# Kernel optimization log

Hardware: AMD Instinct MI355X
Metric: run time of the kernel (lower is better)

The kernel has to match this reference:

```python
import jax, jax.numpy as jnp
import numpy as np

N_NODES = 50000
N_EDGES = 1280000
N_GRAPHS = 64
IN_CH = 6
HID = 64
SLOPE = 0.2  # LeakyReLU negative slope


def _lrelu(x):
    return jax.nn.leaky_relu(x, SLOPE)


def _edge_conv(x, src, dst, W1, b1, W2, b2):
    # PyG EdgeConv: message = nn([x_i, x_j - x_i]); x_i = x[dst], x_j = x[src]; max-aggr onto dst
    xi = x[dst]                                   # [E, F]
    m = jnp.concatenate([xi, x[src] - xi], -1)    # [E, 2F]
    h = _lrelu(_lrelu(m @ W1 + b1) @ W2 + b2)     # [E, H]
    agg = jax.ops.segment_max(h, dst, num_segments=N_NODES)
    return jnp.where(jnp.isneginf(agg), 0.0, agg)  # nodes with no in-edges -> 0


def setup_inputs() -> dict:
    key = jax.random.key(0)
    ks = jax.random.split(key, 12)
    glorot = lambda k, fi, fo: jax.random.normal(k, (fi, fo), jnp.float32) * np.sqrt(2.0 / (fi + fo))
    x = jax.random.normal(ks[0], (N_NODES, IN_CH), jnp.float32)
    edge_index = jax.random.randint(ks[1], (2, N_EDGES), 0, N_NODES, jnp.int64 if jax.config.x64_enabled else jnp.int32)
    batch = jnp.sort(jax.random.randint(ks[2], (N_NODES,), 0, N_GRAPHS))
    return {
        "x": x, "edge_index": edge_index, "batch": batch,
        "W1": glorot(ks[3], 2 * IN_CH, HID), "b1": jnp.zeros((HID,), jnp.float32),
        "W2": glorot(ks[4], HID, HID),       "b2": jnp.zeros((HID,), jnp.float32),
        "W3": glorot(ks[5], 2 * HID, HID),   "b3": jnp.zeros((HID,), jnp.float32),
        "W4": glorot(ks[6], HID, HID),       "b4": jnp.zeros((HID,), jnp.float32),
        "Wc1": glorot(ks[7], 2 * HID, HID),  "bc1": jnp.zeros((HID,), jnp.float32),
        "Wc2": glorot(ks[8], HID, 1),        "bc2": jnp.zeros((1,), jnp.float32),
    }


def reference(x, edge_index, batch, W1, b1, W2, b2, W3, b3, W4, b4, Wc1, bc1, Wc2, bc2):
    src, dst = edge_index[0], edge_index[1]
    h = _edge_conv(x, src, dst, W1, b1, W2, b2)   # [N, H]
    h = _edge_conv(h, src, dst, W3, b3, W4, b4)   # [N, H]
    # global mean + max pool per graph
    cnt = jax.ops.segment_sum(jnp.ones((N_NODES,), h.dtype), batch, num_segments=N_GRAPHS)
    mean_p = jax.ops.segment_sum(h, batch, num_segments=N_GRAPHS) / jnp.clip(cnt, 1.0)[:, None]
    max_p = jax.ops.segment_max(h, batch, num_segments=N_GRAPHS)
    max_p = jnp.where(jnp.isneginf(max_p), 0.0, max_p)
    g = jnp.concatenate([mean_p, max_p], -1)      # [G, 2H]
    logits = _lrelu(g @ Wc1 + bc1) @ Wc2 + bc2    # dropout is identity at inference
    return logits.squeeze(-1)                      # [G]
```

## Files before the change

### kernel.cpp

```cpp
#include <hip/hip_runtime.h>
#include <hip/hip_bf16.h>

#define SLOPE 0.2f
#define NPB 64
#define CAP 2048
#define SUBCAP 384
#define MAXBUCK 1024
#define EPB 4096
#define XF1B 512
#define PPARTS 16

typedef _Float16 f16x8  __attribute__((ext_vector_type(8)));
typedef float    f32x4  __attribute__((ext_vector_type(4)));
typedef unsigned u32;
typedef unsigned u32x4  __attribute__((ext_vector_type(4)));

__device__ __forceinline__ float lrelu(float v) { return fmaxf(v, SLOPE * v); }

__device__ __forceinline__ float lane_bcast(float v, int k) {
    return __int_as_float(__builtin_amdgcn_readlane(__float_as_int(v), k));
}

__device__ __forceinline__ f16x8 lrelu8(f16x8 v) {
    f16x8 s = v * (_Float16)SLOPE;
#if __has_builtin(__builtin_elementwise_max)
    return __builtin_elementwise_max(v, s);
#else
    f16x8 r;
#pragma unroll
    for (int i = 0; i < 8; ++i) r[i] = v[i] > s[i] ? v[i] : s[i];
    return r;
#endif
}

__device__ __forceinline__ void split_f16(float v, _Float16& h, _Float16& l) {
    h = (_Float16)v;
    l = (_Float16)(v - (float)h);
}
__device__ __forceinline__ u32 pack_f16(_Float16 a, _Float16 b) {
    return (u32)__builtin_bit_cast(unsigned short, a) |
           ((u32)__builtin_bit_cast(unsigned short, b) << 16);
}

__global__ void __launch_bounds__(256) scatter_xform1_kernel(
    const int* __restrict__ srcI, const int* __restrict__ dstI,
    int* __restrict__ cursor, u32* __restrict__ pairW,
    int E, int nNodes, int nBuck, int nCntB,
    const float* __restrict__ x,
    const float* __restrict__ W1, const float* __restrict__ b1,
    _Float16* __restrict__ Ph, _Float16* __restrict__ Qh)
{
    if (blockIdx.x < nCntB) {
        __shared__ int cnt4[4][MAXBUCK];
        __shared__ int base[MAXBUCK];
        const int tid = threadIdx.x;
        const int wv  = tid >> 6;
        const int j   = blockIdx.x & 7;
        const int e0 = blockIdx.x * EPB;
        const int e1 = min(e0 + EPB, E);
        const int n4 = (e1 - e0) >> 2;
        const int4* d4 = (const int4*)(dstI + e0);
        const int4* s4 = (const int4*)(srcI + e0);

        for (int b = tid; b < nBuck; b += 256) {
            cnt4[0][b] = 0; cnt4[1][b] = 0; cnt4[2][b] = 0; cnt4[3][b] = 0;
        }
        __syncthreads();
        int* mycnt = cnt4[wv];
        for (int i = tid; i < n4; i += 256) {
            const int4 d = d4[i];
            atomicAdd(&mycnt[d.x >> 6], 1);
            atomicAdd(&mycnt[d.y >> 6], 1);
            atomicAdd(&mycnt[d.z >> 6], 1);
            atomicAdd(&mycnt[d.w >> 6], 1);
        }
        for (int e = e0 + (n4 << 2) + tid; e < e1; e += 256)
            atomicAdd(&mycnt[dstI[e] >> 6], 1);
        __syncthreads();
        for (int b = tid; b < nBuck; b += 256) {
            const int c = (cnt4[0][b] + cnt4[1][b]) + (cnt4[2][b] + cnt4[3][b]);
            base[b] = (c > 0)
                ? ((b * 8 + j) * SUBCAP + min(atomicAdd(&cursor[b * 8 + j], c), SUBCAP))
                : 0;
        }
        __syncthreads();
        for (int b = tid; b < nBuck; b += 256) cnt4[0][b] = 0;
        __syncthreads();
        int* scnt = cnt4[0];
        for (int i = tid; i < n4; i += 256) {
            const int4 d = d4[i];
            const int4 s = s4[i];
            {
                const int b = d.x >> 6;
                const int loc = atomicAdd(&scnt[b], 1);
                pairW[min(base[b] + loc, (b * 8 + j + 1) * SUBCAP - 1)] =
                    ((u32)s.x << 6) | (u32)(d.x & (NPB - 1));
            }
            {
                const int b = d.y >> 6;
                const int loc = atomicAdd(&scnt[b], 1);
                pairW[min(base[b] + loc, (b * 8 + j + 1) * SUBCAP - 1)] =
                    ((u32)s.y << 6) | (u32)(d.y & (NPB - 1));
            }
            {
                const int b = d.z >> 6;
                const int loc = atomicAdd(&scnt[b], 1);
                pairW[min(base[b] + loc, (b * 8 + j + 1) * SUBCAP - 1)] =
                    ((u32)s.z << 6) | (u32)(d.z & (NPB - 1));
            }
            {
                const int b = d.w >> 6;
                const int loc = atomicAdd(&scnt[b], 1);
                pairW[min(base[b] + loc, (b * 8 + j + 1) * SUBCAP - 1)] =
                    ((u32)s.w << 6) | (u32)(d.w & (NPB - 1));
            }
        }
        for (int e = e0 + (n4 << 2) + tid; e < e1; e += 256) {
            const int d = dstI[e];
            const int b = d >> 6;
            const int loc = atomicAdd(&scnt[b], 1);
            pairW[min(base[b] + loc, (b * 8 + j + 1) * SUBCAP - 1)] =
                ((u32)srcI[e] << 6) | (u32)(d & (NPB - 1));
        }
        return;
    }
    const int lane = threadIdx.x & 63;
    const int wave = ((blockIdx.x - nCntB) * 256 + threadIdx.x) >> 6;
    const int nw   = (XF1B * 256) >> 6;

    float wd[6], wb[6];
#pragma unroll
    for (int r = 0; r < 6; ++r) {
        wb[r] = W1[(6 + r) * 64 + lane];
        wd[r] = W1[r * 64 + lane] - wb[r];
    }
    const float bb = b1[lane];
    for (int i = wave; i < nNodes; i += nw) {
        const float* xr = x + (size_t)i * 6;
        float p = bb, q = 0.f;
#pragma unroll
        for (int r = 0; r < 6; ++r) {
            float xv = xr[r];
            p = fmaf(xv, wd[r], p);
            q = fmaf(xv, wb[r], q);
        }
        Ph[(size_t)i * 64 + lane] = (_Float16)p;
        Qh[(size_t)i * 64 + lane] = (_Float16)q;
    }
}

__global__ void __launch_bounds__(256) bucket_sort_kernel(
    const u32* __restrict__ pairW, const int* __restrict__ cursor,
    int2* __restrict__ rowInfo, int* __restrict__ sortedSrc, int nNodes)
{
    __shared__ u32 pairLds[CAP];
    __shared__ int nodeCnt[NPB];
    __shared__ int nodeCur[NPB];
    __shared__ int wcS[8];
    __shared__ int wBase[9];
    const int b   = blockIdx.x;
    const int n0  = b * NPB;
    const int n1  = min(n0 + NPB, nNodes);
    const int tid = threadIdx.x;

    if (tid < NPB) nodeCnt[tid] = 0;
    if (tid < 8) wcS[tid] = min(cursor[b * 8 + tid], SUBCAP);
    __syncthreads();
    if (tid == 0) {
        int acc = 0;
#pragma unroll
        for (int jj = 0; jj < 8; ++jj) { wBase[jj] = acc; acc += wcS[jj]; }
        wBase[8] = acc;
    }
    __syncthreads();

#pragma unroll
    for (int jj = 0; jj < 8; ++jj) {
        const int w0 = (b * 8 + jj) * SUBCAP;
        const int wc = wcS[jj];
        const int d0 = wBase[jj];
        const int nv = wc >> 2;
        const u32x4* p4 = (const u32x4*)(pairW + w0);
        for (int i = tid; i < nv; i += 256) {
            const u32x4 v = p4[i];
            pairLds[d0 + i * 4 + 0] = v[0];
            pairLds[d0 + i * 4 + 1] = v[1];
            pairLds[d0 + i * 4 + 2] = v[2];
            pairLds[d0 + i * 4 + 3] = v[3];
        }
        for (int i = (nv << 2) + tid; i < wc; i += 256)
            pairLds[d0 + i] = pairW[w0 + i];
    }
    __syncthreads();

    const int total = wBase[8];
    for (int i = tid; i < total; i += 256)
        atomicAdd(&nodeCnt[pairLds[i] & (NPB - 1)], 1);
    __syncthreads();
    if (tid < 64) {
        const int c = nodeCnt[tid];
        int inc = c;
#pragma unroll
        for (int off = 1; off < 64; off <<= 1) {
            int t = __shfl_up(inc, off);
            if (tid >= off) inc += t;
        }
        const int st = b * CAP + inc - c;
        nodeCur[tid] = st;
        if (tid < n1 - n0) rowInfo[n0 + tid] = make_int2(st, c);
    }
    __syncthreads();
    for (int i = tid; i < total; i += 256) {
        const u32 w = pairLds[i];
        const int pos = atomicAdd(&nodeCur[w & (NPB - 1)], 1);
        sortedSrc[pos] = (int)(w >> 6);
    }
}

__global__ void __launch_bounds__(256) node_xform2_kernel(
    const _Float16* __restrict__ B1h,
    const float* __restrict__ W3, const float* __restrict__ b3,
    _Float16* __restrict__ Ph, _Float16* __restrict__ Qh, int nNodes)
{
    const int lane = threadIdx.x & 63;
    const int wave = (blockIdx.x * blockDim.x + threadIdx.x) >> 6;
    const int nw   = (gridDim.x * blockDim.x) >> 6;

    float wd[64], wb[64];
#pragma unroll
    for (int k = 0; k < 64; ++k) {
        wb[k] = W3[(64 + k) * 64 + lane];
        wd[k] = W3[k * 64 + lane] - wb[k];
    }
    const float bb = b3[lane];

    for (int i = wave; i < nNodes; i += nw) {
        const float a = (float)B1h[(size_t)i * 64 + lane];
        float p0 = bb, p1 = 0.f, p2 = 0.f, p3 = 0.f;
        float q0 = 0.f, q1 = 0.f, q2 = 0.f, q3 = 0.f;
#pragma unroll
        for (int k = 0; k < 64; k += 4) {
            float a0 = lane_bcast(a, k);
            float a1 = lane_bcast(a, k + 1);
            float a2 = lane_bcast(a, k + 2);
            float a3 = lane_bcast(a, k + 3);
            p0 = fmaf(a0, wd[k],     p0);  q0 = fmaf(a0, wb[k],     q0);
            p1 = fmaf(a1, wd[k + 1], p1);  q1 = fmaf(a1, wb[k + 1], q1);
            p2 = fmaf(a2, wd[k + 2], p2);  q2 = fmaf(a2, wb[k + 2], q2);
            p3 = fmaf(a3, wd[k + 3], p3);  q3 = fmaf(a3, wb[k + 3], q3);
        }
        Ph[(size_t)i * 64 + lane] = (_Float16)((p0 + p1) + (p2 + p3));
        Qh[(size_t)i * 64 + lane] = (_Float16)((q0 + q1) + (q2 + q3));
    }
}


#define COMPUTE32(PA, PB, QA0, QA1, QB0, QB1, M0, M1, M2, M3)                  \
  {                                                                            \
    const f16x8 A00_ = lrelu8((PA) + (QA0));                                   \
    const f16x8 A01_ = lrelu8((PB) + (QA1));                                   \
    const f16x8 A10_ = lrelu8((PA) + (QB0));                                   \
    const f16x8 A11_ = lrelu8((PB) + (QB1));                                   \
    _Pragma("unroll")                                                          \
    for (int nt_ = 0; nt_ < 4; ++nt_) {                                        \
      const f16x8 wh0_ = __builtin_bit_cast(f16x8, wlds[nt_ * 2][lane]);       \
      const f16x8 wh1_ = __builtin_bit_cast(f16x8, wlds[nt_ * 2 + 1][lane]);   \
      const f16x8 wl0_ = __builtin_bit_cast(f16x8, wlds[8 + nt_ * 2][lane]);   \
      const f16x8 wl1_ = __builtin_bit_cast(f16x8, wlds[8 + nt_ * 2 + 1][lane]); \
      f32x4 a_; a_[0] = a_[1] = a_[2] = a_[3] = bc[nt_];                       \
      a_ = __builtin_amdgcn_mfma_f32_16x16x32_f16(A00_, wl0_, a_, 0, 0, 0);    \
      a_ = __builtin_amdgcn_mfma_f32_16x16x32_f16(A00_, wh0_, a_, 0, 0, 0);    \
      a_ = __builtin_amdgcn_mfma_f32_16x16x32_f16(A01_, wl1_, a_, 0, 0, 0);    \
      a_ = __builtin_amdgcn_mfma_f32_16x16x32_f16(A01_, wh1_, a_, 0, 0, 0);    \
      f32x4 c_; c_[0] = c_[1] = c_[2] = c_[3] = bc[nt_];                       \
      c_ = __builtin_amdgcn_mfma_f32_16x16x32_f16(A10_, wl0_, c_, 0, 0, 0);    \
      c_ = __builtin_amdgcn_mfma_f32_16x16x32_f16(A10_, wh0_, c_, 0, 0, 0);    \
      c_ = __builtin_amdgcn_mfma_f32_16x16x32_f16(A11_, wl1_, c_, 0, 0, 0);    \
      c_ = __builtin_amdgcn_mfma_f32_16x16x32_f16(A11_, wh1_, c_, 0, 0, 0);    \
      float m_ = (nt_ == 0) ? (M0) : (nt_ == 1) ? (M1) : (nt_ == 2) ? (M2) : (M3); \
      m_ = fmaxf(fmaxf(fmaxf(a_[0], a_[1]), a_[2]), fmaxf(a_[3], m_));         \
      m_ = fmaxf(fmaxf(fmaxf(c_[0], c_[1]), c_[2]), fmaxf(c_[3], m_));         \
      if (nt_ == 0) (M0) = m_; else if (nt_ == 1) (M1) = m_;                   \
      else if (nt_ == 2) (M2) = m_; else (M3) = m_;                            \
    }                                                                          \
  }

__global__ void __launch_bounds__(256) edge_agg_mfma_kernel(
    const _Float16* __restrict__ Ph, const _Float16* __restrict__ Qh,
    const int2* __restrict__ rowInfo, const int* __restrict__ sortedSrc,
    const float* __restrict__ W, const float* __restrict__ b,
    _Float16* __restrict__ outB, int nNodes)
{
    __shared__ u32x4 wlds[16][64];

    const int tid  = threadIdx.x;
    const int lane = tid & 63;
    const int cn   = lane & 15;
    const int q    = lane >> 4;
    const int wv   = tid >> 6;
    const int wave = (blockIdx.x * 256 + tid) >> 6;
    const int nw   = (gridDim.x * 256) >> 6;

#pragma unroll
    for (int i = 0; i < 4; ++i) {
        const int f    = wv + i * 4;
        const int isLo = f >> 3;
        const int g    = f & 7;
        const int nt   = g >> 1;
        const int ks   = g & 1;
        u32x4 d;
#pragma unroll
        for (int p = 0; p < 4; ++p) {
            float w0 = W[(ks * 32 + q * 8 + 2 * p)     * 64 + nt * 16 + cn];
            float w1 = W[(ks * 32 + q * 8 + 2 * p + 1) * 64 + nt * 16 + cn];
            _Float16 h0, l0, h1, l1;
            split_f16(w0, h0, l0);
            split_f16(w1, h1, l1);
            d[p] = isLo ? pack_f16(l0, l1) : pack_f16(h0, h1);
        }
        wlds[f][lane] = d;
    }
    float bc[4];
#pragma unroll
    for (int nt = 0; nt < 4; ++nt) bc[nt] = b[nt * 16 + cn];
    __syncthreads();

    const int nPairs = (nNodes + 1) >> 1;
    if (wave >= nPairs) return;
    const u32 nClamp = (u32)(nNodes - 1);
    const int nLastN = nNodes - 1;
    const int pLast  = nPairs - 1;

    int rs1, dg1, rs2, dg2;
    u32 sA1, sB1, sA2, sB2;
    int2 riNa, riNb;

    {
        const int n1 = 2 * wave;
        const int2 r1 = rowInfo[n1];
        const int2 r2 = rowInfo[min(n1 + 1, nLastN)];
        rs1 = __builtin_amdgcn_readfirstlane(r1.x);
        dg1 = __builtin_amdgcn_readfirstlane(r1.y);
        rs2 = __builtin_amdgcn_readfirstlane(r2.x);
        dg2 = __builtin_amdgcn_readfirstlane(r2.y);
        const int d1c = max(dg1, 1) - 1;
        const int d2c = max(dg2, 1) - 1;
        sA1 = (u32)sortedSrc[rs1 + min(cn, d1c)];
        sB1 = (u32)sortedSrc[rs1 + min(16 + cn, d1c)];
        sA2 = (u32)sortedSrc[rs2 + min(cn, d2c)];
        sB2 = (u32)sortedSrc[rs2 + min(16 + cn, d2c)];
        const int tn = min(wave + nw, pLast);
        riNa = rowInfo[2 * tn];
        riNb = rowInfo[min(2 * tn + 1, nLastN)];
    }

    for (int t = wave; t < nPairs; t += nw) {
        const int n1 = 2 * t;
        const int n2 = n1 + 1;
        const bool has2 = (n2 < nNodes);
        const int dg2e = has2 ? dg2 : 0;
        const int d1c = max(dg1, 1) - 1;
        const int d2c = max(dg2, 1) - 1;

        const f16x8* QA1 = (const f16x8*)(Qh + (size_t)min(sA1, nClamp) * 64);
        const f16x8* QB1 = (const f16x8*)(Qh + (size_t)min(sB1, nClamp) * 64);
        const f16x8* QA2 = (const f16x8*)(Qh + (size_t)min(sA2, nClamp) * 64);
        const f16x8* QB2 = (const f16x8*)(Qh + (size_t)min(sB2, nClamp) * 64);
        const f16x8 qA1a = QA1[q], qA1b = QA1[4 + q];
        const f16x8 qB1a = QB1[q], qB1b = QB1[4 + q];
        const f16x8 qA2a = QA2[q], qA2b = QA2[4 + q];
        const f16x8 qB2a = QB2[q], qB2b = QB2[4 + q];
        const f16x8* P1 = (const f16x8*)(Ph + (size_t)n1 * 64);
        const f16x8* P2 = (const f16x8*)(Ph + (size_t)min(n2, nLastN) * 64);
        const f16x8 p1A = P1[q], p1B = P1[4 + q];
        const f16x8 p2A = P2[q], p2B = P2[4 + q];

        const int rsN1 = __builtin_amdgcn_readfirstlane(riNa.x);
        const int dgN1 = __builtin_amdgcn_readfirstlane(riNa.y);
        const int rsN2 = __builtin_amdgcn_readfirstlane(riNb.x);
        const int dgN2 = __builtin_amdgcn_readfirstlane(riNb.y);
        const int dN1c = max(dgN1, 1) - 1;
        const int dN2c = max(dgN2, 1) - 1;
        const u32 sNA1 = (u32)sortedSrc[rsN1 + min(cn, dN1c)];
        const u32 sNB1 = (u32)sortedSrc[rsN1 + min(16 + cn, dN1c)];
        const u32 sNA2 = (u32)sortedSrc[rsN2 + min(cn, dN2c)];
        const u32 sNB2 = (u32)sortedSrc[rsN2 + min(16 + cn, dN2c)];
        {
            const int t2 = min(t + 2 * nw, pLast);
            riNa = rowInfo[2 * t2];
            riNb = rowInfo[min(2 * t2 + 1, nLastN)];
        }

        float m10 = -INFINITY, m11 = -INFINITY, m12 = -INFINITY, m13 = -INFINITY;
        float m20 = -INFINITY, m21 = -INFINITY, m22 = -INFINITY, m23 = -INFINITY;
        if (dg1 > 0)  COMPUTE32(p1A, p1B, qA1a, qA1b, qB1a, qB1b, m10, m11, m12, m13);
        if (dg2e > 0) COMPUTE32(p2A, p2B, qA2a, qA2b, qB2a, qB2b, m20, m21, m22, m23);

        const int gmax = max(dg1, dg2e);
        for (int g0 = 32; g0 < gmax; g0 += 32) {
            u32 eA1 = (u32)sortedSrc[rs1 + min(g0 + cn,      d1c)];
            u32 eB1 = (u32)sortedSrc[rs1 + min(g0 + 16 + cn, d1c)];
            u32 eA2 = (u32)sortedSrc[rs2 + min(g0 + cn,      d2c)];
            u32 eB2 = (u32)sortedSrc[rs2 + min(g0 + 16 + cn, d2c)];
            const f16x8* EA1 = (const f16x8*)(Qh + (size_t)min(eA1, nClamp) * 64);
            const f16x8* EB1 = (const f16x8*)(Qh + (size_t)min(eB1, nClamp) * 64);
            const f16x8* EA2 = (const f16x8*)(Qh + (size_t)min(eA2, nClamp) * 64);
            const f16x8* EB2 = (const f16x8*)(Qh + (size_t)min(eB2, nClamp) * 64);
            const f16x8 gA1a = EA1[q], gA1b = EA1[4 + q];
            const f16x8 gB1a = EB1[q], gB1b = EB1[4 + q];
            const f16x8 gA2a = EA2[q], gA2b = EA2[4 + q];
            const f16x8 gB2a = EB2[q], gB2b = EB2[4 + q];
            if (g0 < dg1)  COMPUTE32(p1A, p1B, gA1a, gA1b, gB1a, gB1b, m10, m11, m12, m13);
            if (g0 < dg2e) COMPUTE32(p2A, p2B, gA2a, gA2b, gB2a, gB2b, m20, m21, m22, m23);
        }

        m10 = fmaxf(m10, __shfl_xor(m10, 16)); m10 = fmaxf(m10, __shfl_xor(m10, 32));
        m11 = fmaxf(m11, __shfl_xor(m11, 16)); m11 = fmaxf(m11, __shfl_xor(m11, 32));
        m12 = fmaxf(m12, __shfl_xor(m12, 16)); m12 = fmaxf(m12, __shfl_xor(m12, 32));
        m13 = fmaxf(m13, __shfl_xor(m13, 16)); m13 = fmaxf(m13, __shfl_xor(m13, 32));
        float sel1 = (q < 2) ? ((q == 0) ? m10 : m11) : ((q == 2) ? m12 : m13);
        outB[(size_t)n1 * 64 + q * 16 + cn] =
            (_Float16)((dg1 > 0) ? lrelu(sel1) : 0.0f);

        if (has2) {
            m20 = fmaxf(m20, __shfl_xor(m20, 16)); m20 = fmaxf(m20, __shfl_xor(m20, 32));
            m21 = fmaxf(m21, __shfl_xor(m21, 16)); m21 = fmaxf(m21, __shfl_xor(m21, 32));
            m22 = fmaxf(m22, __shfl_xor(m22, 16)); m22 = fmaxf(m22, __shfl_xor(m22, 32));
            m23 = fmaxf(m23, __shfl_xor(m23, 16)); m23 = fmaxf(m23, __shfl_xor(m23, 32));
            float sel2 = (q < 2) ? ((q == 0) ? m20 : m21) : ((q == 2) ? m22 : m23);
            outB[(size_t)n2 * 64 + q * 16 + cn] =
                (_Float16)((dg2e > 0) ? lrelu(sel2) : 0.0f);
        }

        rs1 = rsN1; dg1 = dgN1; rs2 = rsN2; dg2 = dgN2;
        sA1 = sNA1; sB1 = sNB1; sA2 = sNA2; sB2 = sNB2;
    }
}

__device__ __forceinline__ int lower_bound_i(const int* __restrict__ a, int n, int key)
{
    int lo = 0, hi = n;
    while (lo < hi) {
        int mid = (lo + hi) >> 1;
        if (a[mid] < key) lo = mid + 1; else hi = mid;
    }
    return lo;
}

__global__ void __launch_bounds__(256) pool_kernel(
    const _Float16* __restrict__ Bh, const int* __restrict__ batch,
    float* __restrict__ gpart, int nNodes)
{
    const int gid  = blockIdx.x / PPARTS;
    const int part = blockIdx.x % PPARTS;
    const int c    = threadIdx.x & 63;
    const int wid  = threadIdx.x >> 6;

    const int s = lower_bound_i(batch, nNodes, gid);
    const int e = lower_bound_i(batch, nNodes, gid + 1);
    const int len = e - s;
    const int ps = s + (len * part) / PPARTS;
    const int pe = s + (len * (part + 1)) / PPARTS;

    float sum = 0.f, mx = -INFINITY;
    for (int n = ps + wid; n < pe; n += 4) {
        float v = (float)Bh[(size_t)n * 64 + c];
        sum += v;
        mx = fmaxf(mx, v);
    }
    __shared__ float ssum[4][64];
    __shared__ float smax[4][64];
    ssum[wid][c] = sum;
    smax[wid][c] = mx;
    __syncthreads();
    if (wid == 0) {
        sum = (ssum[0][c] + ssum[1][c]) + (ssum[2][c] + ssum[3][c]);
        mx  = fmaxf(fmaxf(smax[0][c], smax[1][c]), fmaxf(smax[2][c], smax[3][c]));
        float* row = gpart + (size_t)blockIdx.x * 132;
        row[c]      = sum;
        row[64 + c] = mx;
        if (c == 0) row[128] = (float)(pe - ps);
    }
}

__global__ void __launch_bounds__(64) cls_kernel(
    const float* __restrict__ gpart,
    const float* __restrict__ Wc1, const float* __restrict__ bc1,
    const float* __restrict__ Wc2, const float* __restrict__ bc2,
    float* __restrict__ out)
{
    __shared__ float g[128];
    const int gid = blockIdx.x;
    const int c   = threadIdx.x;

    float s = 0.f, m = -INFINITY, cnt = 0.f;
#pragma unroll
    for (int p = 0; p < PPARTS; ++p) {
        const float* row = gpart + (size_t)(gid * PPARTS + p) * 132;
        s += row[c];
        m = fmaxf(m, row[64 + c]);
        cnt += row[128];
    }
    g[c]      = s / fmaxf(cnt, 1.0f);
    g[64 + c] = (cnt > 0.f) ? m : 0.0f;
    __syncthreads();

    float t = bc1[c];
#pragma unroll 8
    for (int k = 0; k < 128; ++k) t = fmaf(g[k], Wc1[k * 64 + c], t);
    t = lrelu(t);
    float p = t * Wc2[c];
#pragma unroll
    for (int off = 32; off > 0; off >>= 1) p += __shfl_down(p, off);
    if (c == 0) out[gid] = p + bc2[0];
}

static inline size_t align_up(size_t v, size_t a) { return (v + a - 1) & ~(a - 1); }

extern "C" void kernel_launch(void* const* d_in, const int* in_sizes, int n_in,
                              void* d_out, int out_size, void* d_ws, size_t ws_size,
                              hipStream_t stream)
{
    const float* x     = (const float*)d_in[0];
    const int*   ei    = (const int*)d_in[1];
    const int*   batch = (const int*)d_in[2];
    const float* W1  = (const float*)d_in[3];
    const float* b1  = (const float*)d_in[4];
    const float* W2  = (const float*)d_in[5];
    const float* b2  = (const float*)d_in[6];
    const float* W3  = (const float*)d_in[7];
    const float* b3  = (const float*)d_in[8];
    const float* W4  = (const float*)d_in[9];
    const float* b4  = (const float*)d_in[10];
    const float* Wc1 = (const float*)d_in[11];
    const float* bc1 = (const float*)d_in[12];
    const float* Wc2 = (const float*)d_in[13];
    const float* bc2 = (const float*)d_in[14];
    float* out = (float*)d_out;

    const int nNodes  = in_sizes[0] / 6;
    const int E       = in_sizes[1] / 2;
    const int nGraphs = out_size;
    const int* srcI = ei;
    const int* dstI = ei + E;
    const int nBuck = (nNodes + NPB - 1) / NPB;
    const int nCntB = (E + EPB - 1) / EPB;

    char* wsp = (char*)d_ws;
    size_t off = 0;
    int*  cursor    = (int*)(wsp + off);   off = align_up(off + (size_t)MAXBUCK * 8 * 4, 256);
    int2* rowInfo   = (int2*)(wsp + off);  off = align_up(off + (size_t)nNodes * 8, 256);
    int*  sortedSrc = (int*)(wsp + off);   off = align_up(off + (size_t)nBuck * CAP * 4, 256);
    u32*  pairW     = (u32*)(wsp + off);   off = align_up(off + (size_t)nBuck * 8 * SUBCAP * 4, 256);
    const size_t nFeat = (size_t)nNodes * 64;
    _Float16* Ph   = (_Float16*)(wsp + off);  off = align_up(off + nFeat * 2, 256);
    _Float16* Qh   = (_Float16*)(wsp + off);  off = align_up(off + nFeat * 2, 256);
    _Float16* B1h  = (_Float16*)(wsp + off);  off = align_up(off + nFeat * 2, 256);
    _Float16* B2h  = (_Float16*)(wsp + off);  off = align_up(off + nFeat * 2, 256);
    float*    gpart= (float*)(wsp + off);     off = align_up(off + (size_t)nGraphs * PPARTS * 132 * 4, 256);
    (void)ws_size;

    (void)hipMemsetAsync(cursor, 0, (size_t)nBuck * 8 * 4, stream);
    scatter_xform1_kernel<<<nCntB + XF1B, 256, 0, stream>>>(
        srcI, dstI, cursor, pairW, E, nNodes, nBuck, nCntB, x, W1, b1, Ph, Qh);
    bucket_sort_kernel<<<nBuck, 256, 0, stream>>>(pairW, cursor, rowInfo,
                                                  sortedSrc, nNodes);

    edge_agg_mfma_kernel<<<2048, 256, 0, stream>>>(Ph, Qh, rowInfo, sortedSrc,
                                                   W2, b2, B1h, nNodes);
    node_xform2_kernel<<<2048, 256, 0, stream>>>(B1h, W3, b3, Ph, Qh, nNodes);
    edge_agg_mfma_kernel<<<2048, 256, 0, stream>>>(Ph, Qh, rowInfo, sortedSrc,
                                                   W4, b4, B2h, nNodes);

    pool_kernel<<<nGraphs * PPARTS, 256, 0, stream>>>(B2h, batch, gpart, nNodes);
    cls_kernel<<<nGraphs, 64, 0, stream>>>(gpart, Wc1, bc1, Wc2, bc2, out);
}
```

Measured before the change: 272.3 us.

## Process four nodes per wave and drop software prefetch in edge aggregation

The edge aggregation kernel now handles four destination nodes per wave iteration instead of two. All 32 neighbor gathers per node are issued up front, which raises memory-level parallelism. The cross-iteration software prefetch of rowInfo and sortedSrc is removed, so index loads now sit on the critical path at the start of each iteration. Register pressure rises with eight gathered row pairs live at once, which may reduce occupancy, and the halved count of work items gives coarser load balance across waves.

```diff
diff --git a/kernel.cpp b/kernel.cpp
--- a/kernel.cpp
+++ b/kernel.cpp
@@ -285,6 +285,18 @@
     }                                                                          \
   }
 
+#define REDUCE_STORE(M0, M1, M2, M3, NODE, DEG)                                \
+  {                                                                            \
+    (M0) = fmaxf((M0), __shfl_xor((M0), 16)); (M0) = fmaxf((M0), __shfl_xor((M0), 32)); \
+    (M1) = fmaxf((M1), __shfl_xor((M1), 16)); (M1) = fmaxf((M1), __shfl_xor((M1), 32)); \
+    (M2) = fmaxf((M2), __shfl_xor((M2), 16)); (M2) = fmaxf((M2), __shfl_xor((M2), 32)); \
+    (M3) = fmaxf((M3), __shfl_xor((M3), 16)); (M3) = fmaxf((M3), __shfl_xor((M3), 32)); \
+    const float sel_ = (q < 2) ? ((q == 0) ? (M0) : (M1))                      \
+                               : ((q == 2) ? (M2) : (M3));                     \
+    outB[(size_t)(NODE) * 64 + q * 16 + cn] =                                  \
+        (_Float16)(((DEG) > 0) ? lrelu(sel_) : 0.0f);                          \
+  }
+
 __global__ void __launch_bounds__(256) edge_agg_mfma_kernel(
     const _Float16* __restrict__ Ph, const _Float16* __restrict__ Qh,
     const int2* __restrict__ rowInfo, const int* __restrict__ sortedSrc,
@@ -325,115 +337,119 @@
     for (int nt = 0; nt < 4; ++nt) bc[nt] = b[nt * 16 + cn];
     __syncthreads();
 
-    const int nPairs = (nNodes + 1) >> 1;
-    if (wave >= nPairs) return;
     const u32 nClamp = (u32)(nNodes - 1);
-    const int nLastN = nNodes - 1;
-    const int pLast  = nPairs - 1;
-
-    int rs1, dg1, rs2, dg2;
-    u32 sA1, sB1, sA2, sB2;
-    int2 riNa, riNb;
-
-    {
-        const int n1 = 2 * wave;
-        const int2 r1 = rowInfo[n1];
-        const int2 r2 = rowInfo[min(n1 + 1, nLastN)];
-        rs1 = __builtin_amdgcn_readfirstlane(r1.x);
-        dg1 = __builtin_amdgcn_readfirstlane(r1.y);
-        rs2 = __builtin_amdgcn_readfirstlane(r2.x);
-        dg2 = __builtin_amdgcn_readfirstlane(r2.y);
+    const int nQuads = (nNodes + 3) >> 2;
+
+    for (int t = wave; t < nQuads; t += nw) {
+        const int n1 = 4 * t;
+        const int n2 = n1 + 1, n3 = n1 + 2, n4 = n1 + 3;
+        const bool has2 = (n2 < nNodes);
+        const bool has3 = (n3 < nNodes);
+        const bool has4 = (n4 < nNodes);
+
+        const int2 ri1 = rowInfo[n1];
+        const int2 ri2 = has2 ? rowInfo[n2] : make_int2(ri1.x, 0);
+        const int2 ri3 = has3 ? rowInfo[n3] : make_int2(ri1.x, 0);
+        const int2 ri4 = has4 ? rowInfo[n4] : make_int2(ri1.x, 0);
+        const int rs1 = __builtin_amdgcn_readfirstlane(ri1.x);
+        const int dg1 = __builtin_amdgcn_readfirstlane(ri1.y);
+        const int rs2 = __builtin_amdgcn_readfirstlane(ri2.x);
+        const int dg2 = __builtin_amdgcn_readfirstlane(ri2.y);
+        const int rs3 = __builtin_amdgcn_readfirstlane(ri3.x);
+        const int dg3 = __builtin_amdgcn_readfirstlane(ri3.y);
+        const int rs4 = __builtin_amdgcn_readfirstlane(ri4.x);
+        const int dg4 = __builtin_amdgcn_readfirstlane(ri4.y);
         const int d1c = max(dg1, 1) - 1;
         const int d2c = max(dg2, 1) - 1;
-        sA1 = (u32)sortedSrc[rs1 + min(cn, d1c)];
-        sB1 = (u32)sortedSrc[rs1 + min(16 + cn, d1c)];
-        sA2 = (u32)sortedSrc[rs2 + min(cn, d2c)];
-        sB2 = (u32)sortedSrc[rs2 + min(16 + cn, d2c)];
-        const int tn = min(wave + nw, pLast);
-        riNa = rowInfo[2 * tn];
-        riNb = rowInfo[min(2 * tn + 1, nLastN)];
-    }
-
-    for (int t = wave; t < nPairs; t += nw) {
-        const int n1 = 2 * t;
-        const int n2 = n1 + 1;
-        const bool has2 = (n2 < nNodes);
-        const int dg2e = has2 ? dg2 : 0;
-        const int d1c = max(dg1, 1) - 1;
-        const int d2c = max(dg2, 1) - 1;
-
-        const f16x8* QA1 = (const f16x8*)(Qh + (size_t)min(sA1, nClamp) * 64);
-        const f16x8* QB1 = (const f16x8*)(Qh + (size_t)min(sB1, nClamp) * 64);
-        const f16x8* QA2 = (const f16x8*)(Qh + (size_t)min(sA2, nClamp) * 64);
-        const f16x8* QB2 = (const f16x8*)(Qh + (size_t)min(sB2, nClamp) * 64);
+        const int d3c = max(dg3, 1) - 1;
+        const int d4c = max(dg4, 1) - 1;
+
+        u32 sA1 = (u32)sortedSrc[rs1 + min(cn,      d1c)];
+        u32 sB1 = (u32)sortedSrc[rs1 + min(16 + cn, d1c)];
+        u32 sA2 = (u32)sortedSrc[rs2 + min(cn,      d2c)];
+        u32 sB2 = (u32)sortedSrc[rs2 + min(16 + cn, d2c)];
+        u32 sA3 = (u32)sortedSrc[rs3 + min(cn,      d3c)];
+        u32 sB3 = (u32)sortedSrc[rs3 + min(16 + cn, d3c)];
+        u32 sA4 = (u32)sortedSrc[rs4 + min(cn,      d4c)];
+        u32 sB4 = (u32)sortedSrc[rs4 + min(16 + cn, d4c)];
+        sA1 = min(sA1, nClamp); sB1 = min(sB1, nClamp);
+        sA2 = min(sA2, nClamp); sB2 = min(sB2, nClamp);
+        sA3 = min(sA3, nClamp); sB3 = min(sB3, nClamp);
+        sA4 = min(sA4, nClamp); sB4 = min(sB4, nClamp);
+
+        const f16x8* QA1 = (const f16x8*)(Qh + (size_t)sA1 * 64);
+        const f16x8* QB1 = (const f16x8*)(Qh + (size_t)sB1 * 64);
+        const f16x8* QA2 = (const f16x8*)(Qh + (size_t)sA2 * 64);
+        const f16x8* QB2 = (const f16x8*)(Qh + (size_t)sB2 * 64);
+        const f16x8* QA3 = (const f16x8*)(Qh + (size_t)sA3 * 64);
+        const f16x8* QB3 = (const f16x8*)(Qh + (size_t)sB3 * 64);
+        const f16x8* QA4 = (const f16x8*)(Qh + (size_t)sA4 * 64);
+        const f16x8* QB4 = (const f16x8*)(Qh + (size_t)sB4 * 64);
         const f16x8 qA1a = QA1[q], qA1b = QA1[4 + q];
         const f16x8 qB1a = QB1[q], qB1b = QB1[4 + q];
         const f16x8 qA2a = QA2[q], qA2b = QA2[4 + q];
         const f16x8 qB2a = QB2[q], qB2b = QB2[4 + q];
+        const f16x8 qA3a = QA3[q], qA3b = QA3[4 + q];
+        const f16x8 qB3a = QB3[q], qB3b = QB3[4 + q];
+        const f16x8 qA4a = QA4[q], qA4b = QA4[4 + q];
+        const f16x8 qB4a = QB4[q], qB4b = QB4[4 + q];
         const f16x8* P1 = (const f16x8*)(Ph + (size_t)n1 * 64);
-        const f16x8* P2 = (const f16x8*)(Ph + (size_t)min(n2, nLastN) * 64);
+        const f16x8* P2 = (const f16x8*)(Ph + (size_t)(has2 ? n2 : n1) * 64);
+        const f16x8* P3 = (const f16x8*)(Ph + (size_t)(has3 ? n3 : n1) * 64);
+        const f16x8* P4 = (const f16x8*)(Ph + (size_t)(has4 ? n4 : n1) * 64);
         const f16x8 p1A = P1[q], p1B = P1[4 + q];
         const f16x8 p2A = P2[q], p2B = P2[4 + q];
-
-        const int rsN1 = __builtin_amdgcn_readfirstlane(riNa.x);
-        const int dgN1 = __builtin_amdgcn_readfirstlane(riNa.y);
-        const int rsN2 = __builtin_amdgcn_readfirstlane(riNb.x);
-        const int dgN2 = __builtin_amdgcn_readfirstlane(riNb.y);
-        const int dN1c = max(dgN1, 1) - 1;
-        const int dN2c = max(dgN2, 1) - 1;
-        const u32 sNA1 = (u32)sortedSrc[rsN1 + min(cn, dN1c)];
-        const u32 sNB1 = (u32)sortedSrc[rsN1 + min(16 + cn, dN1c)];
-        const u32 sNA2 = (u32)sortedSrc[rsN2 + min(cn, dN2c)];
-        const u32 sNB2 = (u32)sortedSrc[rsN2 + min(16 + cn, dN2c)];
-        {
-            const int t2 = min(t + 2 * nw, pLast);
-            riNa = rowInfo[2 * t2];
-            riNb = rowInfo[min(2 * t2 + 1, nLastN)];
-        }
+        const f16x8 p3A = P3[q], p3B = P3[4 + q];
+        const f16x8 p4A = P4[q], p4B = P4[4 + q];
 
         float m10 = -INFINITY, m11 = -INFINITY, m12 = -INFINITY, m13 = -INFINITY;
         float m20 = -INFINITY, m21 = -INFINITY, m22 = -INFINITY, m23 = -INFINITY;
-        if (dg1 > 0)  COMPUTE32(p1A, p1B, qA1a, qA1b, qB1a, qB1b, m10, m11, m12, m13);
-        if (dg2e > 0) COMPUTE32(p2A, p2B, qA2a, qA2b, qB2a, qB2b, m20, m21, m22, m23);
-
-        const int gmax = max(dg1, dg2e);
-        for (int g0 = 32; g0 < gmax; g0 += 32) {
-            u32 eA1 = (u32)sortedSrc[rs1 + min(g0 + cn,      d1c)];
-            u32 eB1 = (u32)sortedSrc[rs1 + min(g0 + 16 + cn, d1c)];
-            u32 eA2 = (u32)sortedSrc[rs2 + min(g0 + cn,      d2c)];
-            u32 eB2 = (u32)sortedSrc[rs2 + min(g0 + 16 + cn, d2c)];
-            const f16x8* EA1 = (const f16x8*)(Qh + (size_t)min(eA1, nClamp) * 64);
-            const f16x8* EB1 = (const f16x8*)(Qh + (size_t)min(eB1, nClamp) * 64);
-            const f16x8* EA2 = (const f16x8*)(Qh + (size_t)min(eA2, nClamp) * 64);
-            const f16x8* EB2 = (const f16x8*)(Qh + (size_t)min(eB2, nClamp) * 64);
+        float m30 = -INFINITY, m31 = -INFINITY, m32 = -INFINITY, m33 = -INFINITY;
+        float m40 = -INFINITY, m41 = -INFINITY, m42 = -INFINITY, m43 = -INFINITY;
+        if (dg1 > 0) COMPUTE32(p1A, p1B, qA1a, qA1b, qB1a, qB1b, m10, m11, m12, m13);
+        if (dg2 > 0) COMPUTE32(p2A, p2B, qA2a, qA2b, qB2a, qB2b, m20, m21, m22, m23);
+        if (dg3 > 0) COMPUTE32(p3A, p3B, qA3a, qA3b, qB3a, qB3b, m30, m31, m32, m33);
+        if (dg4 > 0) COMPUTE32(p4A, p4B, qA4a, qA4b, qB4a, qB4b, m40, m41, m42, m43);
+
+        const int gmax12 = max(dg1, dg2);
+        for (int g0 = 32; g0 < gmax12; g0 += 32) {
+            u32 eA1 = min((u32)sortedSrc[rs1 + min(g0 + cn,      d1c)], nClamp);
+            u32 eB1 = min((u32)sortedSrc[rs1 + min(g0 + 16 + cn, d1c)], nClamp);
+            u32 eA2 = min((u32)sortedSrc[rs2 + min(g0 + cn,      d2c)], nClamp);
+            u32 eB2 = min((u32)sortedSrc[rs2 + min(g0 + 16 + cn, d2c)], nClamp);
+            const f16x8* EA1 = (const f16x8*)(Qh + (size_t)eA1 * 64);
+            const f16x8* EB1 = (const f16x8*)(Qh + (size_t)eB1 * 64);
+            const f16x8* EA2 = (const f16x8*)(Qh + (size_t)eA2 * 64);
+            const f16x8* EB2 = (const f16x8*)(Qh + (size_t)eB2 * 64);
             const f16x8 gA1a = EA1[q], gA1b = EA1[4 + q];
             const f16x8 gB1a = EB1[q], gB1b = EB1[4 + q];
             const f16x8 gA2a = EA2[q], gA2b = EA2[4 + q];
             const f16x8 gB2a = EB2[q], gB2b = EB2[4 + q];
-            if (g0 < dg1)  COMPUTE32(p1A, p1B, gA1a, gA1b, gB1a, gB1b, m10, m11, m12, m13);
-            if (g0 < dg2e) COMPUTE32(p2A, p2B, gA2a, gA2b, gB2a, gB2b, m20, m21, m22, m23);
-        }
-
-        m10 = fmaxf(m10, __shfl_xor(m10, 16)); m10 = fmaxf(m10, __shfl_xor(m10, 32));
-        m11 = fmaxf(m11, __shfl_xor(m11, 16)); m11 = fmaxf(m11, __shfl_xor(m11, 32));
-        m12 = fmaxf(m12, __shfl_xor(m12, 16)); m12 = fmaxf(m12, __shfl_xor(m12, 32));
-        m13 = fmaxf(m13, __shfl_xor(m13, 16)); m13 = fmaxf(m13, __shfl_xor(m13, 32));
-        float sel1 = (q < 2) ? ((q == 0) ? m10 : m11) : ((q == 2) ? m12 : m13);
-        outB[(size_t)n1 * 64 + q * 16 + cn] =
-            (_Float16)((dg1 > 0) ? lrelu(sel1) : 0.0f);
-
-        if (has2) {
-            m20 = fmaxf(m20, __shfl_xor(m20, 16)); m20 = fmaxf(m20, __shfl_xor(m20, 32));
-            m21 = fmaxf(m21, __shfl_xor(m21, 16)); m21 = fmaxf(m21, __shfl_xor(m21, 32));
-            m22 = fmaxf(m22, __shfl_xor(m22, 16)); m22 = fmaxf(m22, __shfl_xor(m22, 32));
-            m23 = fmaxf(m23, __shfl_xor(m23, 16)); m23 = fmaxf(m23, __shfl_xor(m23, 32));
-            float sel2 = (q < 2) ? ((q == 0) ? m20 : m21) : ((q == 2) ? m22 : m23);
-            outB[(size_t)n2 * 64 + q * 16 + cn] =
-                (_Float16)((dg2e > 0) ? lrelu(sel2) : 0.0f);
-        }
-
-        rs1 = rsN1; dg1 = dgN1; rs2 = rsN2; dg2 = dgN2;
-        sA1 = sNA1; sB1 = sNB1; sA2 = sNA2; sB2 = sNB2;
+            if (g0 < dg1) COMPUTE32(p1A, p1B, gA1a, gA1b, gB1a, gB1b, m10, m11, m12, m13);
+            if (g0 < dg2) COMPUTE32(p2A, p2B, gA2a, gA2b, gB2a, gB2b, m20, m21, m22, m23);
+        }
+        const int gmax34 = max(dg3, dg4);
+        for (int g0 = 32; g0 < gmax34; g0 += 32) {
+            u32 eA3 = min((u32)sortedSrc[rs3 + min(g0 + cn,      d3c)], nClamp);
+            u32 eB3 = min((u32)sortedSrc[rs3 + min(g0 + 16 + cn, d3c)], nClamp);
+            u32 eA4 = min((u32)sortedSrc[rs4 + min(g0 + cn,      d4c)], nClamp);
+            u32 eB4 = min((u32)sortedSrc[rs4 + min(g0 + 16 + cn, d4c)], nClamp);
+            const f16x8* EA3 = (const f16x8*)(Qh + (size_t)eA3 * 64);
+            const f16x8* EB3 = (const f16x8*)(Qh + (size_t)eB3 * 64);
+            const f16x8* EA4 = (const f16x8*)(Qh + (size_t)eA4 * 64);
+            const f16x8* EB4 = (const f16x8*)(Qh + (size_t)eB4 * 64);
+            const f16x8 gA3a = EA3[q], gA3b = EA3[4 + q];
+            const f16x8 gB3a = EB3[q], gB3b = EB3[4 + q];
+            const f16x8 gA4a = EA4[q], gA4b = EA4[4 + q];
+            const f16x8 gB4a = EB4[q], gB4b = EB4[4 + q];
+            if (g0 < dg3) COMPUTE32(p3A, p3B, gA3a, gA3b, gB3a, gB3b, m30, m31, m32, m33);
+            if (g0 < dg4) COMPUTE32(p4A, p4B, gA4a, gA4b, gB4a, gB4b, m40, m41, m42, m43);
+        }
+
+        REDUCE_STORE(m10, m11, m12, m13, n1, dg1);
+        if (has2) REDUCE_STORE(m20, m21, m22, m23, n2, dg2);
+        if (has3) REDUCE_STORE(m30, m31, m32, m33, n3, dg3);
+        if (has4) REDUCE_STORE(m40, m41, m42, m43, n4, dg4);
     }
 }
 
```

Measured after the change: 275.1 us. No clear change (+1.0%).
